# Kernel tuning notes

Hardware: AMD Instinct MI355X
Metric: run time of the kernel (lower is better)

The kernel has to match this reference:

```python
import math
import jax, jax.numpy as jnp
import numpy as np

B, T, H, E, K, F = 4, 4096, 512, 8, 2, 2048
CAP_FACTOR, ROUND_TO = 0.3125, 128


def _capacity(num_tokens):
    cap = math.ceil(CAP_FACTOR * num_tokens)
    cap = ROUND_TO * math.ceil(cap / ROUND_TO)
    return max(1, min(cap, num_tokens))


def setup_inputs() -> dict:
    key = jax.random.key(0)
    k0, k1, k2, k3 = jax.random.split(key, 4)
    x = jax.random.normal(k0, (B, T, H), jnp.float32)
    router_w = jax.random.normal(k1, (H, E), jnp.float32) * 0.02
    w1 = jax.random.normal(k2, (E, H, F), jnp.float32) * (1.0 / np.sqrt(H))
    b1 = jnp.zeros((E, F), jnp.float32)
    w2 = jax.random.normal(k3, (E, F, H), jnp.float32) * (1.0 / np.sqrt(F))
    b2 = jnp.zeros((E, H), jnp.float32)
    return {"x": x, "router_w": router_w, "w1": w1, "b1": b1, "w2": w2, "b2": b2}


def reference(x, router_w, w1, b1, w2, b2):
    Bc, Tc, Hc = x.shape
    n = Bc * Tc
    cap = _capacity(n)  # static: 5120
    flat = x.reshape(n, Hc)

    # Router + top-k selection (fp32 logits, softmax over selected logits)
    logits = (flat @ router_w).astype(jnp.float32)          # [n, E]
    sel_logits, expert_idx = jax.lax.top_k(logits, K)       # [n, K]
    weights = jax.nn.softmax(sel_logits, axis=-1)           # [n, K]

    # Flatten (token, k) assignments and sort by expert (stable)
    fe = expert_idx.reshape(-1).astype(jnp.int32)           # [n*K]
    fw = weights.reshape(-1)
    tok = jnp.broadcast_to(jnp.arange(n, dtype=jnp.int32)[:, None], expert_idx.shape).reshape(-1)
    order = jnp.argsort(fe)  # jax sort is stable
    se, st, sw = fe[order], tok[order], fw[order]

    # Per-expert slot index; assignments beyond capacity are dropped
    counts = jnp.bincount(se, length=E)                     # [E]
    offsets = (jnp.cumsum(counts) - counts).astype(jnp.int32)
    slot = jnp.arange(se.shape[0], dtype=jnp.int32) - offsets[se]
    keep = slot < cap
    sw = jnp.where(keep, sw, 0.0)                           # dropped tokens contribute 0

    # Pack into fixed-capacity expert buffers (out-of-range slots dropped)
    sx = flat[st]                                           # [n*K, H]
    expert_inputs = jnp.zeros((E, cap, Hc), flat.dtype).at[se, slot].set(sx, mode='drop')

    # Grouped expert MLP: Dense(F) -> GELU -> Dense(H)
    h = jax.nn.gelu(jnp.einsum('ech,ehf->ecf', expert_inputs, w1) + b1[:, None, :])
    out = jnp.einsum('ecf,efh->ech', h, w2) + b2[:, None, :]

    # Zero invalid (unused) slots
    clipped = jnp.minimum(counts, cap)
    valid = (jnp.arange(cap, dtype=jnp.int32)[None, :] < clipped[:, None])[..., None]
    out = jnp.where(valid, out, 0)

    # Scatter-combine weighted expert outputs back to tokens
    slot_c = jnp.minimum(slot, cap - 1)                     # dropped rows have weight 0
    gathered = out[se, slot_c] * sw[:, None].astype(out.dtype)
    combined = jnp.zeros((n, Hc), out.dtype).at[st].add(gathered)
    return combined.reshape(Bc, Tc, Hc)
```

## Files before the change

### kernel.cpp

```cpp
#include <hip/hip_runtime.h>
#include <hip/hip_bf16.h>

#define NTOK 16384
#define HD   512
#define ED   8
#define FD   2048
#define CAP  5120
#define NA   32768

typedef __bf16 bf16x8 __attribute__((ext_vector_type(8)));
typedef float  f32x4  __attribute__((ext_vector_type(4)));

static constexpr size_t OFF_EIDX = 0;
static constexpr size_t OFF_WGT  = 131072;
static constexpr size_t OFF_STOK = 262144;
static constexpr size_t OFF_ASLOT= 425984;
static constexpr size_t OFF_ECNT = 557056;
static constexpr size_t OFF_W2T  = 1u << 20;
static constexpr size_t OFF_H    = OFF_W2T + (size_t)ED*HD*FD*2;
static constexpr size_t OFF_W1T  = OFF_H   + (size_t)ED*CAP*FD*2;
static constexpr size_t OFF_XBF  = OFF_W1T + (size_t)ED*FD*HD*2;
static constexpr size_t OFF_EOUT = OFF_XBF + (size_t)NTOK*HD*2;

__device__ __forceinline__ unsigned short f2bf(float f) {
    __bf16 b = (__bf16)f;
    return __builtin_bit_cast(unsigned short, b);
}
__device__ __forceinline__ unsigned short f2h(float f) {
    _Float16 h = (_Float16)f;
    return __builtin_bit_cast(unsigned short, h);
}
__device__ __forceinline__ float h2f(unsigned short u) {
    return (float)__builtin_bit_cast(_Float16, u);
}

__device__ __forceinline__ float gelu_fast(float v) {
    const float t = v * v;
    const float u = v * fmaf(t, 0.0713548214f, 1.5957691216f);
    const float e = __expf(-u);
    return v * __builtin_amdgcn_rcpf(1.f + e);
}

__device__ __forceinline__ void gl16(const unsigned short* g, unsigned short* l) {
    __builtin_amdgcn_global_load_lds(
        (const __attribute__((address_space(1))) unsigned int*)(const void*)g,
        (__attribute__((address_space(3))) unsigned int*)(void*)l, 16, 0, 0);
}

__global__ __launch_bounds__(256) void transpose_cast_kernel(
    const float* __restrict__ in, unsigned short* __restrict__ out, int R, int C)
{
    __shared__ unsigned short tile[32][33];
    const int e = blockIdx.z;
    in  += (size_t)e * R * C;
    out += (size_t)e * R * C;
    const int r0 = blockIdx.y * 32, c0 = blockIdx.x * 32;
    const int tr = threadIdx.x >> 3, tc = (threadIdx.x & 7) * 4;
    const float4 v = *(const float4*)(in + (size_t)(r0 + tr) * C + c0 + tc);
    tile[tr][tc + 0] = f2bf(v.x);
    tile[tr][tc + 1] = f2bf(v.y);
    tile[tr][tc + 2] = f2bf(v.z);
    tile[tr][tc + 3] = f2bf(v.w);
    __syncthreads();
    ushort4 o;
    o.x = tile[tc + 0][tr]; o.y = tile[tc + 1][tr];
    o.z = tile[tc + 2][tr]; o.w = tile[tc + 3][tr];
    *(ushort4*)(out + (size_t)(c0 + tr) * R + r0 + tc) = o;
}

__global__ __launch_bounds__(256) void router_kernel(
    const float* __restrict__ x, const float* __restrict__ rw,
    int* __restrict__ eidx, float* __restrict__ wgt,
    unsigned short* __restrict__ xbf)
{
    __shared__ float rws[HD * ED];
    const int tid = threadIdx.x;
    for (int i = tid * 4; i < HD * ED; i += 256 * 4)
        *(float4*)(rws + i) = *(const float4*)(rw + i);
    __syncthreads();

    const int wid = tid >> 6, lane = tid & 63;
    const int t = blockIdx.x * 4 + wid;
    const float* xr = x + (size_t)t * HD;

    float acc[ED];
#pragma unroll
    for (int e = 0; e < ED; e++) acc[e] = 0.f;

    float4 xv0 = *(const float4*)(xr + lane * 8);
    float4 xv1 = *(const float4*)(xr + lane * 8 + 4);
    float xv[8] = {xv0.x, xv0.y, xv0.z, xv0.w, xv1.x, xv1.y, xv1.z, xv1.w};

    union { unsigned short us[8]; uint4 v; } pk;
#pragma unroll
    for (int j = 0; j < 8; j++) pk.us[j] = f2bf(xv[j]);
    *(uint4*)(xbf + (size_t)t * HD + lane * 8) = pk.v;

#pragma unroll
    for (int j = 0; j < 8; j++) {
        const int h = lane * 8 + j;
#pragma unroll
        for (int e = 0; e < ED; e++) acc[e] += xv[j] * rws[h * ED + e];
    }
#pragma unroll
    for (int off = 32; off >= 1; off >>= 1) {
#pragma unroll
        for (int e = 0; e < ED; e++) acc[e] += __shfl_down(acc[e], off);
    }
    if (lane == 0) {
        int e0 = 0; float l0 = acc[0];
        for (int e = 1; e < ED; e++) if (acc[e] > l0) { l0 = acc[e]; e0 = e; }
        int e1 = 0; float l1 = -1e30f;
        for (int e = 0; e < ED; e++) {
            if (e == e0) continue;
            if (acc[e] > l1) { l1 = acc[e]; e1 = e; }
        }
        const float ex = expf(l1 - l0);
        const float inv = 1.f / (1.f + ex);
        eidx[t * 2 + 0] = e0;  eidx[t * 2 + 1] = e1;
        wgt [t * 2 + 0] = inv; wgt [t * 2 + 1] = ex * inv;
    }
}

__global__ __launch_bounds__(1024) void scan_kernel(
    const int* __restrict__ eidx,
    int* __restrict__ stok, int* __restrict__ aslot, int* __restrict__ ecnt)
{
    __shared__ int running[ED];
    __shared__ int wcnt[16][ED];
    const int tid = threadIdx.x;

    for (int i = tid; i < ED * CAP; i += 1024) stok[i] = -1;
    if (tid < ED) running[tid] = 0;
    __syncthreads();

    const int lane = tid & 63, wid = tid >> 6;
    const unsigned long long below = (1ull << lane) - 1ull;

    for (int c = 0; c < NA / 1024; c++) {
        const int a = c * 1024 + tid;
        const int e = eidx[a];
        int myrank = 0;
#pragma unroll
        for (int ee = 0; ee < ED; ee++) {
            unsigned long long m = __ballot(e == ee);
            if (ee == e) myrank = __popcll(m & below);
            if (lane == 0) wcnt[wid][ee] = __popcll(m);
        }
        __syncthreads();
        int woff = 0;
        for (int ww = 0; ww < wid; ww++) woff += wcnt[ww][e];
        const int slot = running[e] + woff + myrank;
        if (slot < CAP) {
            stok[e * CAP + slot] = a >> 1;
            aslot[a] = slot;
        } else {
            aslot[a] = -1;
        }
        __syncthreads();
        if (tid < ED) {
            int tot = 0;
            for (int ww = 0; ww < 16; ww++) tot += wcnt[ww][tid];
            running[tid] += tot;
        }
        __syncthreads();
    }
    if (tid < ED) ecnt[tid] = running[tid] < CAP ? running[tid] : CAP;
}

template<int KD, int ND, int NT, bool G1>
__global__ __launch_bounds__(256) void gemm_mfma(
    const unsigned short* __restrict__ Abase,
    const unsigned short* __restrict__ Bt,
    const float* __restrict__ bias,
    const int* __restrict__ stok,
    const int* __restrict__ ecnt,
    unsigned short* __restrict__ hout)
{
    constexpr int BUFE = 128 * 32;
    __shared__ __align__(16) unsigned short As[2 * BUFE];
    __shared__ __align__(16) unsigned short Bs[2 * BUFE];

    const int tid = threadIdx.x;
    const int e  = blockIdx.x & 7;
    const int g  = blockIdx.x >> 3;
    const int n0 = (g % NT) * 128;
    const int m0 = (g / NT) * 128;

    if (m0 >= ecnt[e]) return;

    const int lane = tid & 63;
    const int wid  = tid >> 6;

    const int rsub = lane >> 2;
    const int csw  = (lane & 3) ^ ((rsub >> 1) & 3);

    const unsigned short *ag0, *ag1, *bg0, *bg1;
    {
        const int R0 = (wid * 2 + 0) * 16 + rsub;
        const int R1 = (wid * 2 + 1) * 16 + rsub;
        size_t a0, a1;
        if constexpr (G1) {
            const int t0 = stok[e * CAP + m0 + R0];
            const int t1 = stok[e * CAP + m0 + R1];
            a0 = (size_t)(t0 >= 0 ? t0 : 0);
            a1 = (size_t)(t1 >= 0 ? t1 : 0);
        } else {
            a0 = (size_t)(e * CAP + m0 + R0);
            a1 = (size_t)(e * CAP + m0 + R1);
        }
        ag0 = Abase + a0 * KD + csw * 8;
        ag1 = Abase + a1 * KD + csw * 8;
        bg0 = Bt + ((size_t)e * ND + n0 + R0) * KD + csw * 8;
        bg1 = Bt + ((size_t)e * ND + n0 + R1) * KD + csw * 8;
    }
    unsigned short* lA = As + (wid * 2) * 512;
    unsigned short* lB = Bs + (wid * 2) * 512;

    const int wrow = (wid & 1) * 64;
    const int wcol = (wid >> 1) * 64;
    const int l15  = lane & 15;
    const int quad = lane >> 4;
    const int xq   = quad ^ ((l15 >> 1) & 3);
    const int fA   = (wrow + l15) * 32 + xq * 8;
    const int fB   = (wcol + l15) * 32 + xq * 8;

    f32x4 acc[4][4];
#pragma unroll
    for (int i = 0; i < 4; i++)
#pragma unroll
        for (int j = 0; j < 4; j++) acc[i][j] = (f32x4)0.f;

#define STAGE(B, KC)                                                           \
    {                                                                          \
        gl16(ag0 + (KC), lA + (B) * BUFE);                                     \
        gl16(ag1 + (KC), lA + (B) * BUFE + 512);                               \
        gl16(bg0 + (KC), lB + (B) * BUFE);                                     \
        gl16(bg1 + (KC), lB + (B) * BUFE + 512);                               \
    }

#define COMPUTE(B)                                                             \
    {                                                                          \
        const unsigned short* Ab = As + (B) * BUFE;                            \
        const unsigned short* Bb = Bs + (B) * BUFE;                            \
        bf16x8 af[4], bfv[4];                                                  \
        _Pragma("unroll")                                                      \
        for (int i = 0; i < 4; i++) af[i]  = *(const bf16x8*)(Ab + fA + i * 512); \
        _Pragma("unroll")                                                      \
        for (int j = 0; j < 4; j++) bfv[j] = *(const bf16x8*)(Bb + fB + j * 512); \
        _Pragma("unroll")                                                      \
        for (int i = 0; i < 4; i++)                                            \
            _Pragma("unroll")                                                  \
            for (int j = 0; j < 4; j++)                                        \
                acc[i][j] = __builtin_amdgcn_mfma_f32_16x16x32_bf16(           \
                    bfv[j], af[i], acc[i][j], 0, 0, 0);                        \
    }

    STAGE(0, 0);
    __syncthreads();

    for (int kc = 0; kc <= KD - 128; kc += 64) {
        STAGE(1, kc + 32);
        COMPUTE(0);
        __syncthreads();
        STAGE(0, kc + 64);
        COMPUTE(1);
        __syncthreads();
    }
    STAGE(1, KD - 32);
    COMPUTE(0);
    __syncthreads();
    COMPUTE(1);
#undef STAGE
#undef COMPUTE

#pragma unroll
    for (int i = 0; i < 4; i++) {
        unsigned short* hrow = hout
            + ((size_t)e * CAP + m0 + wrow + i * 16 + l15) * ND
            + n0 + wcol + quad * 4;
#pragma unroll
        for (int j = 0; j < 4; j++) {
            const float4 b4 = *(const float4*)(
                bias + (size_t)e * ND + n0 + wcol + j * 16 + quad * 4);
            const float v0 = acc[i][j][0] + b4.x;
            const float v1 = acc[i][j][1] + b4.y;
            const float v2 = acc[i][j][2] + b4.z;
            const float v3 = acc[i][j][3] + b4.w;
            ushort4 o;
            if constexpr (G1) {
                o.x = f2bf(gelu_fast(v0)); o.y = f2bf(gelu_fast(v1));
                o.z = f2bf(gelu_fast(v2)); o.w = f2bf(gelu_fast(v3));
            } else {
                o.x = f2h(v0); o.y = f2h(v1); o.z = f2h(v2); o.w = f2h(v3);
            }
            *(ushort4*)(hrow + j * 16) = o;
        }
    }
}

__global__ __launch_bounds__(256) void combine_kernel(
    const unsigned short* __restrict__ eout,
    const int* __restrict__ eidx, const int* __restrict__ aslot,
    const float* __restrict__ wgt, float* __restrict__ out)
{
    const int tid = threadIdx.x;
    const int t  = blockIdx.x * 2 + (tid >> 7);
    const int h0 = (tid & 127) * 4;
    float r0 = 0.f, r1 = 0.f, r2 = 0.f, r3 = 0.f;
#pragma unroll
    for (int k = 0; k < 2; k++) {
        const int a = t * 2 + k;
        const int s = aslot[a];
        if (s >= 0) {
            const float w = wgt[a];
            const int e = eidx[a];
            const ushort4 v = *(const ushort4*)(eout + ((size_t)e * CAP + s) * HD + h0);
            r0 += w * h2f(v.x); r1 += w * h2f(v.y);
            r2 += w * h2f(v.z); r3 += w * h2f(v.w);
        }
    }
    float4 o; o.x = r0; o.y = r1; o.z = r2; o.w = r3;
    *(float4*)(out + (size_t)t * HD + h0) = o;
}

extern "C" void kernel_launch(void* const* d_in, const int* in_sizes, int n_in,
                              void* d_out, int out_size, void* d_ws, size_t ws_size,
                              hipStream_t stream)
{
    const float* x  = (const float*)d_in[0];
    const float* rw = (const float*)d_in[1];
    const float* w1 = (const float*)d_in[2];
    const float* b1 = (const float*)d_in[3];
    const float* w2 = (const float*)d_in[4];
    const float* b2 = (const float*)d_in[5];
    float* out = (float*)d_out;

    char* ws = (char*)d_ws;
    int*   eidx  = (int*)  (ws + OFF_EIDX);
    float* wgt   = (float*)(ws + OFF_WGT);
    int*   stok  = (int*)  (ws + OFF_STOK);
    int*   aslot = (int*)  (ws + OFF_ASLOT);
    int*   ecnt  = (int*)  (ws + OFF_ECNT);
    unsigned short* w2t  = (unsigned short*)(ws + OFF_W2T);
    unsigned short* hbuf = (unsigned short*)(ws + OFF_H);
    unsigned short* w1t  = (unsigned short*)(ws + OFF_W1T);
    unsigned short* xbf  = (unsigned short*)(ws + OFF_XBF);
    unsigned short* eout = (unsigned short*)(ws + OFF_EOUT);

    transpose_cast_kernel<<<dim3(FD / 32, HD / 32, ED), 256, 0, stream>>>(w1, w1t, HD, FD);
    transpose_cast_kernel<<<dim3(HD / 32, FD / 32, ED), 256, 0, stream>>>(w2, w2t, FD, HD);
    router_kernel<<<NTOK / 4, 256, 0, stream>>>(x, rw, eidx, wgt, xbf);
    scan_kernel<<<1, 1024, 0, stream>>>(eidx, stok, aslot, ecnt);

    gemm_mfma<HD, FD, FD/128, true>
        <<<8 * (FD/128) * (CAP/128), 256, 0, stream>>>(
        xbf, w1t, b1, stok, ecnt, hbuf);

    gemm_mfma<FD, HD, HD/128, false>
        <<<8 * (HD/128) * (CAP/128), 256, 0, stream>>>(
        hbuf, w2t, b2, nullptr, ecnt, eout);

    combine_kernel<<<NTOK / 2, 256, 0, stream>>>(eout, eidx, aslot, wgt, out);
}
```

Baseline: 464.6 us.

## Triple-buffer LDS in expert GEMM with explicit vmcnt-based waits

Moves the MFMA GEMM main loop from double to triple buffering of the A and B LDS tiles. Two tiles are prefetched ahead, and explicit s_waitcnt vmcnt counts plus raw s_barrier replace __syncthreads, so global loads stay in flight across barriers. The aim is to hide global-to-LDS load latency better. In exchange LDS use rises by half, which may lower occupancy, and correctness now depends on the hand-set wait counts.

New measurement: 466.3 us. No clear change (+0.4%).

```diff
diff --git a/kernel.cpp b/kernel.cpp
--- a/kernel.cpp
+++ b/kernel.cpp
@@ -178,8 +178,9 @@
     unsigned short* __restrict__ hout)
 {
     constexpr int BUFE = 128 * 32;
-    __shared__ __align__(16) unsigned short As[2 * BUFE];
-    __shared__ __align__(16) unsigned short Bs[2 * BUFE];
+    constexpr int NTK  = KD / 32;
+    __shared__ __align__(16) unsigned short As[3 * BUFE];
+    __shared__ __align__(16) unsigned short Bs[3 * BUFE];
 
     const int tid = threadIdx.x;
     const int e  = blockIdx.x & 7;
@@ -231,18 +232,18 @@
 #pragma unroll
         for (int j = 0; j < 4; j++) acc[i][j] = (f32x4)0.f;
 
-#define STAGE(B, KC)                                                           \
+#define STAGE(BB, KC)                                                          \
     {                                                                          \
-        gl16(ag0 + (KC), lA + (B) * BUFE);                                     \
-        gl16(ag1 + (KC), lA + (B) * BUFE + 512);                               \
-        gl16(bg0 + (KC), lB + (B) * BUFE);                                     \
-        gl16(bg1 + (KC), lB + (B) * BUFE + 512);                               \
-    }
-
-#define COMPUTE(B)                                                             \
+        gl16(ag0 + (KC), lA + (BB));                                           \
+        gl16(ag1 + (KC), lA + (BB) + 512);                                     \
+        gl16(bg0 + (KC), lB + (BB));                                           \
+        gl16(bg1 + (KC), lB + (BB) + 512);                                     \
+    }
+
+#define COMPUTE(BB)                                                            \
     {                                                                          \
-        const unsigned short* Ab = As + (B) * BUFE;                            \
-        const unsigned short* Bb = Bs + (B) * BUFE;                            \
+        const unsigned short* Ab = As + (BB);                                  \
+        const unsigned short* Bb = Bs + (BB);                                  \
         bf16x8 af[4], bfv[4];                                                  \
         _Pragma("unroll")                                                      \
         for (int i = 0; i < 4; i++) af[i]  = *(const bf16x8*)(Ab + fA + i * 512); \
@@ -257,20 +258,37 @@
     }
 
     STAGE(0, 0);
-    __syncthreads();
-
-    for (int kc = 0; kc <= KD - 128; kc += 64) {
-        STAGE(1, kc + 32);
-        COMPUTE(0);
-        __syncthreads();
-        STAGE(0, kc + 64);
-        COMPUTE(1);
-        __syncthreads();
-    }
-    STAGE(1, KD - 32);
-    COMPUTE(0);
-    __syncthreads();
-    COMPUTE(1);
+    STAGE(BUFE, 32);
+    STAGE(2 * BUFE, 64);
+
+    int bb = 0;
+    int kc_next = 96;
+    for (int t = 0; t < NTK - 3; ++t) {
+        asm volatile("s_waitcnt vmcnt(8)" ::: "memory");
+        __builtin_amdgcn_s_barrier();
+        asm volatile("" ::: "memory");
+        COMPUTE(bb);
+        asm volatile("s_waitcnt lgkmcnt(0)" ::: "memory");
+        __builtin_amdgcn_s_barrier();
+        asm volatile("" ::: "memory");
+        STAGE(bb, kc_next);
+        kc_next += 32;
+        bb = (bb == 2 * BUFE) ? 0 : bb + BUFE;
+    }
+    asm volatile("s_waitcnt vmcnt(8)" ::: "memory");
+    __builtin_amdgcn_s_barrier();
+    asm volatile("" ::: "memory");
+    COMPUTE(bb);
+    bb = (bb == 2 * BUFE) ? 0 : bb + BUFE;
+    asm volatile("s_waitcnt vmcnt(4)" ::: "memory");
+    __builtin_amdgcn_s_barrier();
+    asm volatile("" ::: "memory");
+    COMPUTE(bb);
+    bb = (bb == 2 * BUFE) ? 0 : bb + BUFE;
+    asm volatile("s_waitcnt vmcnt(0)" ::: "memory");
+    __builtin_amdgcn_s_barrier();
+    asm volatile("" ::: "memory");
+    COMPUTE(bb);
 #undef STAGE
 #undef COMPUTE
 
```

## Triple-buffer GEMM K-loop with register prefetch and parallelize routing scan

Applied to the files above, without the earlier changes.

The grouped GEMM kernel moves from a double-buffered LDS pipeline with full __syncthreads to a three-stage ring. It uses explicit vmcnt/lgkmcnt waits, raw barriers, and register double-buffering of fragments, so LDS reads for the next step overlap the MFMAs of the current one, with s_setprio around the MFMA bursts. Separately, the routing scan kernel now counts per-wave expert occupancy for all chunks up front and computes offsets with a wave-level prefix scan. This removes three block barriers per chunk. The changes raise LDS use per block and depend on hand-counted vmcnt values being correct for the async global-to-LDS loads.

Result: slower. 487.2 us (+4.9%).

```diff
diff --git a/kernel.cpp b/kernel.cpp
--- a/kernel.cpp
+++ b/kernel.cpp
@@ -126,16 +126,43 @@
     const int* __restrict__ eidx,
     int* __restrict__ stok, int* __restrict__ aslot, int* __restrict__ ecnt)
 {
-    __shared__ int running[ED];
-    __shared__ int wcnt[16][ED];
+    __shared__ int wcnt[32][16][ED];
+    __shared__ int woff[32][16][ED];
     const int tid = threadIdx.x;
-
-    for (int i = tid; i < ED * CAP; i += 1024) stok[i] = -1;
-    if (tid < ED) running[tid] = 0;
-    __syncthreads();
-
     const int lane = tid & 63, wid = tid >> 6;
     const unsigned long long below = (1ull << lane) - 1ull;
+
+    for (int i = tid; i < ED * CAP; i += 1024) stok[i] = -1;
+
+    for (int c = 0; c < NA / 1024; c++) {
+        const int e = eidx[c * 1024 + tid];
+#pragma unroll
+        for (int ee = 0; ee < ED; ee++) {
+            unsigned long long m = __ballot(e == ee);
+            if (lane == 0) wcnt[c][wid][ee] = __popcll(m);
+        }
+    }
+    __syncthreads();
+
+    if (wid < ED) {
+        const int e = wid;
+        int carry = 0;
+#pragma unroll
+        for (int r = 0; r < 8; r++) {
+            const int idx = r * 64 + lane;
+            const int v = wcnt[idx >> 4][idx & 15][e];
+            int s = v;
+#pragma unroll
+            for (int off = 1; off < 64; off <<= 1) {
+                int u = __shfl_up(s, off);
+                if (lane >= off) s += u;
+            }
+            woff[idx >> 4][idx & 15][e] = carry + s - v;
+            carry += __shfl(s, 63);
+        }
+        if (lane == 0) ecnt[e] = carry < CAP ? carry : CAP;
+    }
+    __syncthreads();
 
     for (int c = 0; c < NA / 1024; c++) {
         const int a = c * 1024 + tid;
@@ -145,27 +172,15 @@
         for (int ee = 0; ee < ED; ee++) {
             unsigned long long m = __ballot(e == ee);
             if (ee == e) myrank = __popcll(m & below);
-            if (lane == 0) wcnt[wid][ee] = __popcll(m);
-        }
-        __syncthreads();
-        int woff = 0;
-        for (int ww = 0; ww < wid; ww++) woff += wcnt[ww][e];
-        const int slot = running[e] + woff + myrank;
+        }
+        const int slot = woff[c][wid][e] + myrank;
         if (slot < CAP) {
             stok[e * CAP + slot] = a >> 1;
             aslot[a] = slot;
         } else {
             aslot[a] = -1;
         }
-        __syncthreads();
-        if (tid < ED) {
-            int tot = 0;
-            for (int ww = 0; ww < 16; ww++) tot += wcnt[ww][tid];
-            running[tid] += tot;
-        }
-        __syncthreads();
-    }
-    if (tid < ED) ecnt[tid] = running[tid] < CAP ? running[tid] : CAP;
+    }
 }
 
 template<int KD, int ND, int NT, bool G1>
@@ -178,8 +193,9 @@
     unsigned short* __restrict__ hout)
 {
     constexpr int BUFE = 128 * 32;
-    __shared__ __align__(16) unsigned short As[2 * BUFE];
-    __shared__ __align__(16) unsigned short Bs[2 * BUFE];
+    constexpr int NTK  = KD / 32;
+    __shared__ __align__(16) unsigned short As[3 * BUFE];
+    __shared__ __align__(16) unsigned short Bs[3 * BUFE];
 
     const int tid = threadIdx.x;
     const int e  = blockIdx.x & 7;
@@ -231,48 +247,95 @@
 #pragma unroll
         for (int j = 0; j < 4; j++) acc[i][j] = (f32x4)0.f;
 
-#define STAGE(B, KC)                                                           \
+    bf16x8 afA[4], bfA[4], afB[4], bfB[4];
+
+#define STAGE(SO, KC)                                                          \
     {                                                                          \
-        gl16(ag0 + (KC), lA + (B) * BUFE);                                     \
-        gl16(ag1 + (KC), lA + (B) * BUFE + 512);                               \
-        gl16(bg0 + (KC), lB + (B) * BUFE);                                     \
-        gl16(bg1 + (KC), lB + (B) * BUFE + 512);                               \
-    }
-
-#define COMPUTE(B)                                                             \
+        gl16(ag0 + (KC), lA + (SO));                                           \
+        gl16(ag1 + (KC), lA + (SO) + 512);                                     \
+        gl16(bg0 + (KC), lB + (SO));                                           \
+        gl16(bg1 + (KC), lB + (SO) + 512);                                     \
+    }
+
+#define DSREAD(RA, RB, SO)                                                     \
     {                                                                          \
-        const unsigned short* Ab = As + (B) * BUFE;                            \
-        const unsigned short* Bb = Bs + (B) * BUFE;                            \
-        bf16x8 af[4], bfv[4];                                                  \
         _Pragma("unroll")                                                      \
-        for (int i = 0; i < 4; i++) af[i]  = *(const bf16x8*)(Ab + fA + i * 512); \
+        for (int i = 0; i < 4; i++) RA[i] = *(const bf16x8*)(As + (SO) + fA + i * 512); \
         _Pragma("unroll")                                                      \
-        for (int j = 0; j < 4; j++) bfv[j] = *(const bf16x8*)(Bb + fB + j * 512); \
+        for (int j = 0; j < 4; j++) RB[j] = *(const bf16x8*)(Bs + (SO) + fB + j * 512); \
+    }
+
+#define MFMA16(RA, RB)                                                         \
+    {                                                                          \
+        __builtin_amdgcn_s_setprio(1);                                         \
         _Pragma("unroll")                                                      \
         for (int i = 0; i < 4; i++)                                            \
             _Pragma("unroll")                                                  \
             for (int j = 0; j < 4; j++)                                        \
                 acc[i][j] = __builtin_amdgcn_mfma_f32_16x16x32_bf16(           \
-                    bfv[j], af[i], acc[i][j], 0, 0, 0);                        \
-    }
+                    RB[j], RA[i], acc[i][j], 0, 0, 0);                         \
+        __builtin_amdgcn_s_setprio(0);                                         \
+    }
+
+#define CLOSE_STEP                                                             \
+    asm volatile("s_waitcnt lgkmcnt(0)" ::: "memory");                         \
+    __builtin_amdgcn_s_barrier();                                              \
+    asm volatile("" ::: "memory");
+
+#define OPEN_STEP(VMSTR)                                                       \
+    asm volatile(VMSTR ::: "memory");                                          \
+    __builtin_amdgcn_s_barrier();                                              \
+    asm volatile("" ::: "memory");
 
     STAGE(0, 0);
-    __syncthreads();
-
-    for (int kc = 0; kc <= KD - 128; kc += 64) {
-        STAGE(1, kc + 32);
-        COMPUTE(0);
-        __syncthreads();
-        STAGE(0, kc + 64);
-        COMPUTE(1);
-        __syncthreads();
-    }
-    STAGE(1, KD - 32);
-    COMPUTE(0);
-    __syncthreads();
-    COMPUTE(1);
+    STAGE(BUFE, 32);
+    STAGE(2 * BUFE, 64);
+    OPEN_STEP("s_waitcnt vmcnt(8)");
+    DSREAD(afA, bfA, 0);
+    CLOSE_STEP
+
+    int sSt = 0;
+    int sRd = BUFE;
+    int kcS = 96;
+    for (int t = 0; t <= NTK - 6; t += 2) {
+        STAGE(sSt, kcS);
+        OPEN_STEP("s_waitcnt vmcnt(8)");
+        DSREAD(afB, bfB, sRd);
+        MFMA16(afA, bfA);
+        CLOSE_STEP
+        sSt = (sSt == 2 * BUFE) ? 0 : sSt + BUFE;
+        sRd = (sRd == 2 * BUFE) ? 0 : sRd + BUFE;
+        kcS += 32;
+        STAGE(sSt, kcS);
+        OPEN_STEP("s_waitcnt vmcnt(8)");
+        DSREAD(afA, bfA, sRd);
+        MFMA16(afB, bfB);
+        CLOSE_STEP
+        sSt = (sSt == 2 * BUFE) ? 0 : sSt + BUFE;
+        sRd = (sRd == 2 * BUFE) ? 0 : sRd + BUFE;
+        kcS += 32;
+    }
+    STAGE(sSt, (NTK - 1) * 32);
+    OPEN_STEP("s_waitcnt vmcnt(8)");
+    DSREAD(afB, bfB, sRd);
+    MFMA16(afA, bfA);
+    CLOSE_STEP
+    sRd = (sRd == 2 * BUFE) ? 0 : sRd + BUFE;
+    OPEN_STEP("s_waitcnt vmcnt(4)");
+    DSREAD(afA, bfA, sRd);
+    MFMA16(afB, bfB);
+    CLOSE_STEP
+    sRd = (sRd == 2 * BUFE) ? 0 : sRd + BUFE;
+    OPEN_STEP("s_waitcnt vmcnt(0)");
+    DSREAD(afB, bfB, sRd);
+    MFMA16(afA, bfA);
+    CLOSE_STEP
+    MFMA16(afB, bfB);
 #undef STAGE
-#undef COMPUTE
+#undef DSREAD
+#undef MFMA16
+#undef CLOSE_STEP
+#undef OPEN_STEP
 
 #pragma unroll
     for (int i = 0; i < 4; i++) {
```

## Use 256x256 GEMM tiles with 8 waves, ping-pong pipeline, and two-pass scan

Applied to the files above, without the earlier changes.

The expert GEMMs move from 128x128 tiles on 4 waves to 256x256 tiles on 512 threads, with a K-step of 64 in quadrant-staged double buffers. Shared-memory reads, global-to-LDS loads and MFMA quadrants are interleaved with explicit barriers, vmcnt waits and setprio to overlap memory with compute and raise data reuse per tile. The single-block scan is also restructured: it counts all chunks first, does a parallel prefix per expert with wave shuffles, then assigns slots without per-chunk barriers. Larger tiles mean fewer blocks (occupancy and tail-effect risk) and rely on hand-tuned wait counts for correctness.

Measured after the change: 484.6 us. +4.3%, slower.

```diff
diff --git a/kernel.cpp b/kernel.cpp
--- a/kernel.cpp
+++ b/kernel.cpp
@@ -126,16 +126,43 @@
     const int* __restrict__ eidx,
     int* __restrict__ stok, int* __restrict__ aslot, int* __restrict__ ecnt)
 {
-    __shared__ int running[ED];
-    __shared__ int wcnt[16][ED];
+    __shared__ int wcnt[32][16][ED];
+    __shared__ int woff[32][16][ED];
     const int tid = threadIdx.x;
-
-    for (int i = tid; i < ED * CAP; i += 1024) stok[i] = -1;
-    if (tid < ED) running[tid] = 0;
-    __syncthreads();
-
     const int lane = tid & 63, wid = tid >> 6;
     const unsigned long long below = (1ull << lane) - 1ull;
+
+    for (int i = tid; i < ED * CAP; i += 1024) stok[i] = -1;
+
+    for (int c = 0; c < NA / 1024; c++) {
+        const int e = eidx[c * 1024 + tid];
+#pragma unroll
+        for (int ee = 0; ee < ED; ee++) {
+            unsigned long long m = __ballot(e == ee);
+            if (lane == 0) wcnt[c][wid][ee] = __popcll(m);
+        }
+    }
+    __syncthreads();
+
+    if (wid < ED) {
+        const int e = wid;
+        int carry = 0;
+#pragma unroll
+        for (int r = 0; r < 8; r++) {
+            const int idx = r * 64 + lane;
+            const int v = wcnt[idx >> 4][idx & 15][e];
+            int s = v;
+#pragma unroll
+            for (int off = 1; off < 64; off <<= 1) {
+                int u = __shfl_up(s, off);
+                if (lane >= off) s += u;
+            }
+            woff[idx >> 4][idx & 15][e] = carry + s - v;
+            carry += __shfl(s, 63);
+        }
+        if (lane == 0) ecnt[e] = carry < CAP ? carry : CAP;
+    }
+    __syncthreads();
 
     for (int c = 0; c < NA / 1024; c++) {
         const int a = c * 1024 + tid;
@@ -145,31 +172,19 @@
         for (int ee = 0; ee < ED; ee++) {
             unsigned long long m = __ballot(e == ee);
             if (ee == e) myrank = __popcll(m & below);
-            if (lane == 0) wcnt[wid][ee] = __popcll(m);
-        }
-        __syncthreads();
-        int woff = 0;
-        for (int ww = 0; ww < wid; ww++) woff += wcnt[ww][e];
-        const int slot = running[e] + woff + myrank;
+        }
+        const int slot = woff[c][wid][e] + myrank;
         if (slot < CAP) {
             stok[e * CAP + slot] = a >> 1;
             aslot[a] = slot;
         } else {
             aslot[a] = -1;
         }
-        __syncthreads();
-        if (tid < ED) {
-            int tot = 0;
-            for (int ww = 0; ww < 16; ww++) tot += wcnt[ww][tid];
-            running[tid] += tot;
-        }
-        __syncthreads();
-    }
-    if (tid < ED) ecnt[tid] = running[tid] < CAP ? running[tid] : CAP;
-}
-
-template<int KD, int ND, int NT, bool G1>
-__global__ __launch_bounds__(256) void gemm_mfma(
+    }
+}
+
+template<int KD, int ND, int NTN, bool G1>
+__global__ __launch_bounds__(512) void gemm_mfma(
     const unsigned short* __restrict__ Abase,
     const unsigned short* __restrict__ Bt,
     const float* __restrict__ bias,
@@ -177,116 +192,151 @@
     const int* __restrict__ ecnt,
     unsigned short* __restrict__ hout)
 {
-    constexpr int BUFE = 128 * 32;
-    __shared__ __align__(16) unsigned short As[2 * BUFE];
-    __shared__ __align__(16) unsigned short Bs[2 * BUFE];
+    constexpr int NTK = KD / 64;
+    __shared__ __align__(16) unsigned short As[2 * 2 * 128 * 64];
+    __shared__ __align__(16) unsigned short Bs[2 * 2 * 128 * 64];
 
     const int tid = threadIdx.x;
     const int e  = blockIdx.x & 7;
     const int g  = blockIdx.x >> 3;
-    const int n0 = (g % NT) * 128;
-    const int m0 = (g / NT) * 128;
+    const int n0 = (g % NTN) * 256;
+    const int m0 = (g / NTN) * 256;
 
     if (m0 >= ecnt[e]) return;
 
-    const int lane = tid & 63;
-    const int wid  = tid >> 6;
-
-    const int rsub = lane >> 2;
-    const int csw  = (lane & 3) ^ ((rsub >> 1) & 3);
-
-    const unsigned short *ag0, *ag1, *bg0, *bg1;
-    {
-        const int R0 = (wid * 2 + 0) * 16 + rsub;
-        const int R1 = (wid * 2 + 1) * 16 + rsub;
-        size_t a0, a1;
-        if constexpr (G1) {
-            const int t0 = stok[e * CAP + m0 + R0];
-            const int t1 = stok[e * CAP + m0 + R1];
-            a0 = (size_t)(t0 >= 0 ? t0 : 0);
-            a1 = (size_t)(t1 >= 0 ? t1 : 0);
-        } else {
-            a0 = (size_t)(e * CAP + m0 + R0);
-            a1 = (size_t)(e * CAP + m0 + R1);
-        }
-        ag0 = Abase + a0 * KD + csw * 8;
-        ag1 = Abase + a1 * KD + csw * 8;
-        bg0 = Bt + ((size_t)e * ND + n0 + R0) * KD + csw * 8;
-        bg1 = Bt + ((size_t)e * ND + n0 + R1) * KD + csw * 8;
-    }
-    unsigned short* lA = As + (wid * 2) * 512;
-    unsigned short* lB = Bs + (wid * 2) * 512;
-
-    const int wrow = (wid & 1) * 64;
-    const int wcol = (wid >> 1) * 64;
-    const int l15  = lane & 15;
-    const int quad = lane >> 4;
-    const int xq   = quad ^ ((l15 >> 1) & 3);
-    const int fA   = (wrow + l15) * 32 + xq * 8;
-    const int fB   = (wcol + l15) * 32 + xq * 8;
-
-    f32x4 acc[4][4];
-#pragma unroll
-    for (int i = 0; i < 4; i++)
+    const int lane = tid & 63, wid = tid >> 6;
+    const int wm = wid & 1, wn = wid >> 1;
+
+    const int srow = lane >> 3;
+    const int csw  = ((lane & 7) ^ srow) * 8;
+    unsigned int aOff[2][2], bOff[2][2];
+#pragma unroll
+    for (int h = 0; h < 2; h++) {
+#pragma unroll
+        for (int p = 0; p < 2; p++) {
+            const int R = h * 128 + (wid * 2 + p) * 8 + srow;
+            unsigned int arow;
+            if constexpr (G1) {
+                const int t = stok[e * CAP + m0 + R];
+                arow = (unsigned int)(t >= 0 ? t : 0);
+            } else {
+                arow = (unsigned int)(e * CAP + m0 + R);
+            }
+            aOff[h][p] = arow * KD + csw;
+            bOff[h][p] = (unsigned int)((e * ND + n0 + R) * KD) + csw;
+        }
+    }
+
+    const int l15 = lane & 15, quad = lane >> 4;
+    const int x0  = quad ^ (l15 & 7);
+    const int aRd = wm * 8192 + l15 * 64 + x0 * 8;
+    const int bRd = (wn >> 1) * 8192 + (wn & 1) * 4096 + l15 * 64 + x0 * 8;
+
+    f32x4 acc[8][4];
+#pragma unroll
+    for (int i = 0; i < 8; i++)
 #pragma unroll
         for (int j = 0; j < 4; j++) acc[i][j] = (f32x4)0.f;
 
-#define STAGE(B, KC)                                                           \
-    {                                                                          \
-        gl16(ag0 + (KC), lA + (B) * BUFE);                                     \
-        gl16(ag1 + (KC), lA + (B) * BUFE + 512);                               \
-        gl16(bg0 + (KC), lB + (B) * BUFE);                                     \
-        gl16(bg1 + (KC), lB + (B) * BUFE + 512);                               \
-    }
-
-#define COMPUTE(B)                                                             \
-    {                                                                          \
-        const unsigned short* Ab = As + (B) * BUFE;                            \
-        const unsigned short* Bb = Bs + (B) * BUFE;                            \
-        bf16x8 af[4], bfv[4];                                                  \
+    bf16x8 aLO[4][2], aHI[4][2], bHIr[2][2], bL[2][2];
+
+#define FENCE asm volatile("" ::: "memory")
+#define BARR  { FENCE; __builtin_amdgcn_s_barrier(); FENCE; }
+
+#define ST_A(D, H, KC)                                                         \
+    { gl16(Abase + aOff[H][0] + (KC), As + ((D)*2+(H))*8192 + (wid*2+0)*512);  \
+      gl16(Abase + aOff[H][1] + (KC), As + ((D)*2+(H))*8192 + (wid*2+1)*512); }
+#define ST_B(D, H, KC)                                                         \
+    { gl16(Bt + bOff[H][0] + (KC), Bs + ((D)*2+(H))*8192 + (wid*2+0)*512);     \
+      gl16(Bt + bOff[H][1] + (KC), Bs + ((D)*2+(H))*8192 + (wid*2+1)*512); }
+
+#define RD_A(DST, D, QM)                                                       \
+    { _Pragma("unroll")                                                        \
+      for (int f = 0; f < 4; f++) {                                            \
+        DST[f][0] = *(const bf16x8*)(As + (D)*16384 + (QM)*4096 + f*1024 + aRd);        \
+        DST[f][1] = *(const bf16x8*)(As + (D)*16384 + (QM)*4096 + f*1024 + (aRd^32)); } }
+#define RD_B(DST, D, QN)                                                       \
+    { _Pragma("unroll")                                                        \
+      for (int j = 0; j < 2; j++) {                                            \
+        DST[j][0] = *(const bf16x8*)(Bs + (D)*16384 + (QN)*2048 + j*1024 + bRd);        \
+        DST[j][1] = *(const bf16x8*)(Bs + (D)*16384 + (QN)*2048 + j*1024 + (bRd^32)); } }
+
+#define MFMA16(QM, QN, AF, BF)                                                 \
+    { __builtin_amdgcn_s_setprio(1);                                           \
+      _Pragma("unroll")                                                        \
+      for (int fi = 0; fi < 4; fi++)                                           \
         _Pragma("unroll")                                                      \
-        for (int i = 0; i < 4; i++) af[i]  = *(const bf16x8*)(Ab + fA + i * 512); \
-        _Pragma("unroll")                                                      \
-        for (int j = 0; j < 4; j++) bfv[j] = *(const bf16x8*)(Bb + fB + j * 512); \
-        _Pragma("unroll")                                                      \
-        for (int i = 0; i < 4; i++)                                            \
-            _Pragma("unroll")                                                  \
-            for (int j = 0; j < 4; j++)                                        \
-                acc[i][j] = __builtin_amdgcn_mfma_f32_16x16x32_bf16(           \
-                    bfv[j], af[i], acc[i][j], 0, 0, 0);                        \
-    }
-
-    STAGE(0, 0);
-    __syncthreads();
-
-    for (int kc = 0; kc <= KD - 128; kc += 64) {
-        STAGE(1, kc + 32);
-        COMPUTE(0);
-        __syncthreads();
-        STAGE(0, kc + 64);
-        COMPUTE(1);
-        __syncthreads();
-    }
-    STAGE(1, KD - 32);
-    COMPUTE(0);
-    __syncthreads();
-    COMPUTE(1);
-#undef STAGE
-#undef COMPUTE
-
-#pragma unroll
-    for (int i = 0; i < 4; i++) {
+        for (int fj = 0; fj < 2; fj++) {                                       \
+            acc[(QM)*4+fi][(QN)*2+fj] = __builtin_amdgcn_mfma_f32_16x16x32_bf16( \
+                BF[fj][0], AF[fi][0], acc[(QM)*4+fi][(QN)*2+fj], 0, 0, 0);     \
+            acc[(QM)*4+fi][(QN)*2+fj] = __builtin_amdgcn_mfma_f32_16x16x32_bf16( \
+                BF[fj][1], AF[fi][1], acc[(QM)*4+fi][(QN)*2+fj], 0, 0, 0);     \
+        }                                                                      \
+      __builtin_amdgcn_s_setprio(0); }
+
+#define GROUP(D, KC1, KC2)                                                     \
+     BARR;                                                             \
+    RD_B(bHIr, (D), 1);                                                        \
+    ST_A(1-(D), 1, (KC1));                                                     \
+    MFMA16(0, 0, aLO, bL);                                                     \
+     BARR;                                                             \
+    RD_A(aHI, (D), 1);                                                         \
+    ST_B(1-(D), 0, (KC1));                                                     \
+    MFMA16(0, 1, aLO, bHIr);                                                   \
+     BARR;                                                             \
+    ST_B((D), 1, (KC2));                                                       \
+    MFMA16(1, 1, aHI, bHIr);                                                   \
+     asm volatile("s_waitcnt vmcnt(2)" ::: "memory");                  \
+    BARR;                                                                      \
+    RD_A(aLO, 1-(D), 0);                                                       \
+    ST_A((D), 0, (KC2));                                                       \
+    MFMA16(1, 0, aHI, bL);                                                     \
+    RD_B(bL, 1-(D), 0);
+
+    ST_A(0, 0, 0);
+    ST_A(0, 1, 0);
+    ST_B(0, 0, 0);
+    ST_B(0, 1, 0);
+    ST_B(1, 1, 64);
+    ST_A(1, 0, 64);
+    asm volatile("s_waitcnt vmcnt(4)" ::: "memory");
+    BARR;
+    RD_A(aLO, 0, 0);
+    RD_B(bL, 0, 0);
+
+#pragma unroll 1
+    for (int G = 0; G < NTK; G += 2) {
+        const int t1 = G + 1;
+        const int t2 = (G + 2 >= NTK) ? 0 : G + 2;
+        const int t3 = (G + 3 >= NTK) ? G + 3 - NTK : G + 3;
+        GROUP(0, t1 * 64, t2 * 64)
+        GROUP(1, t2 * 64, t3 * 64)
+    }
+    asm volatile("s_waitcnt vmcnt(0)" ::: "memory");
+#undef GROUP
+#undef MFMA16
+#undef RD_A
+#undef RD_B
+#undef ST_A
+#undef ST_B
+#undef BARR
+#undef FENCE
+
+    float4 bb4[4];
+#pragma unroll
+    for (int j = 0; j < 4; j++)
+        bb4[j] = *(const float4*)(bias + (size_t)e * ND + n0 + wn * 64 + j * 16 + quad * 4);
+#pragma unroll
+    for (int i = 0; i < 8; i++) {
         unsigned short* hrow = hout
-            + ((size_t)e * CAP + m0 + wrow + i * 16 + l15) * ND
-            + n0 + wcol + quad * 4;
+            + ((size_t)e * CAP + m0 + wm * 128 + i * 16 + l15) * ND
+            + n0 + wn * 64 + quad * 4;
 #pragma unroll
         for (int j = 0; j < 4; j++) {
-            const float4 b4 = *(const float4*)(
-                bias + (size_t)e * ND + n0 + wcol + j * 16 + quad * 4);
-            const float v0 = acc[i][j][0] + b4.x;
-            const float v1 = acc[i][j][1] + b4.y;
-            const float v2 = acc[i][j][2] + b4.z;
-            const float v3 = acc[i][j][3] + b4.w;
+            const float v0 = acc[i][j][0] + bb4[j].x;
+            const float v1 = acc[i][j][1] + bb4[j].y;
+            const float v2 = acc[i][j][2] + bb4[j].z;
+            const float v3 = acc[i][j][3] + bb4[j].w;
             ushort4 o;
             if constexpr (G1) {
                 o.x = f2bf(gelu_fast(v0)); o.y = f2bf(gelu_fast(v1));
@@ -353,12 +403,12 @@
     router_kernel<<<NTOK / 4, 256, 0, stream>>>(x, rw, eidx, wgt, xbf);
     scan_kernel<<<1, 1024, 0, stream>>>(eidx, stok, aslot, ecnt);
 
-    gemm_mfma<HD, FD, FD/128, true>
-        <<<8 * (FD/128) * (CAP/128), 256, 0, stream>>>(
+    gemm_mfma<HD, FD, FD/256, true>
+        <<<8 * (FD/256) * (CAP/256), 512, 0, stream>>>(
         xbf, w1t, b1, stok, ecnt, hbuf);
 
-    gemm_mfma<FD, HD, HD/128, false>
-        <<<8 * (HD/128) * (CAP/128), 256, 0, stream>>>(
+    gemm_mfma<FD, HD, HD/256, false>
+        <<<8 * (HD/256) * (CAP/256), 512, 0, stream>>>(
         hbuf, w2t, b2, nullptr, ecnt, eout);
 
     combine_kernel<<<NTOK / 2, 256, 0, stream>>>(eout, eidx, aslot, wgt, out);
```
